# Optimization experiments

Measured on AMD Instinct MI355X. Metric: run time of the kernel, lower is better.

Reference implementation:

```python
import jax, jax.numpy as jnp
import numpy as np

M = 81920          # total triples = 1024 groups * (2*39 + 2)
NB = 39            # num_neighbor
TOTAL_ENT = 14541
TOTAL_REL = 237
D = 100            # embedding_dim == BiLSTM_input_size
H = 100            # lstm hidden (== hidden_size1)
ALPHA = 0.2
MU = 0.001


def _lstm_seq(x, Wih, Whh, b):
    """x: [B,T,D] -> hidden states [B,T,H]. PyTorch gate order i,f,g,o."""
    B = x.shape[0]
    Hh = Whh.shape[1]
    def step(carry, xt):
        h, c = carry
        g = xt @ Wih.T + h @ Whh.T + b
        i, f, gg, o = jnp.split(g, 4, axis=-1)
        c = jax.nn.sigmoid(f) * c + jax.nn.sigmoid(i) * jnp.tanh(gg)
        h = jax.nn.sigmoid(o) * jnp.tanh(c)
        return (h, c), h
    init = (jnp.zeros((B, Hh), x.dtype), jnp.zeros((B, Hh), x.dtype))
    _, hs = jax.lax.scan(step, init, jnp.swapaxes(x, 0, 1))
    return jnp.swapaxes(hs, 0, 1)


def _gat(inp, W, a_vec):
    """inp: [B,N,F] -> [B,F]. GAT-style attention against node 0, thresholded by MU."""
    h = jnp.einsum('bnf,fo->bno', inp, W)
    a0 = jnp.broadcast_to(h[:, :1, :], h.shape)           # node-0 features repeated
    e = jax.nn.leaky_relu(jnp.concatenate([h, a0], axis=-1) @ a_vec, ALPHA)  # [B,N,1]
    att = jax.nn.softmax(e, axis=1)
    att = jnp.maximum(att - MU, 0.0)                      # (x + |x|)/2 == relu(x)
    return jnp.einsum('bnl,bnf->bf', att, h)              # l == 1


def setup_inputs():
    key = jax.random.key(0)
    ks = jax.random.split(key, 20)
    u = 6.0 / np.sqrt(D)        # embedding uniform range as in the module
    sl = 1.0 / np.sqrt(H)       # pytorch LSTM init scale
    F6 = 6 * H
    def uni(k, shape, s):
        return jax.random.uniform(k, shape, minval=-s, maxval=s, dtype=jnp.float32)
    xav1 = 1.414 * np.sqrt(2.0 / (F6 + F6))
    xav2 = 1.414 * np.sqrt(2.0 / (H + H))
    return {
        'batch_h': jax.random.randint(ks[0], (M,), 0, TOTAL_ENT),
        'batch_r': jax.random.randint(ks[1], (M,), 0, TOTAL_REL),
        'batch_t': jax.random.randint(ks[2], (M,), 0, TOTAL_ENT),
        'ent_emb': uni(ks[3], (TOTAL_ENT, D), u),
        'rel_emb': uni(ks[4], (TOTAL_REL, D), u),
        'ent_emb1': uni(ks[5], (TOTAL_ENT, D), u),
        'rel_emb1': uni(ks[6], (TOTAL_REL, D), u),
        'Wih_f': uni(ks[7], (4 * H, D), sl),
        'Whh_f': uni(ks[8], (4 * H, H), sl),
        'b_f': uni(ks[9], (4 * H,), sl),
        'Wih_b': uni(ks[10], (4 * H, D), sl),
        'Whh_b': uni(ks[11], (4 * H, H), sl),
        'b_b': uni(ks[12], (4 * H,), sl),
        'Wih_p': uni(ks[13], (4 * H, D), sl),
        'Whh_p': uni(ks[14], (4 * H, H), sl),
        'b_p': uni(ks[15], (4 * H,), sl),
        'W_att1': jax.random.normal(ks[16], (F6, F6), dtype=jnp.float32) * xav1,
        'a_att1': jax.random.normal(ks[17], (2 * F6, 1), dtype=jnp.float32) * 0.05,
        'W_att2': jax.random.normal(ks[18], (H, H), dtype=jnp.float32) * xav2,
        'a_att2': jax.random.normal(ks[19], (2 * H, 1), dtype=jnp.float32) * 0.05,
    }


def reference(batch_h, batch_r, batch_t, ent_emb, rel_emb, ent_emb1, rel_emb1,
              Wih_f, Whh_f, b_f, Wih_b, Whh_b, b_b, Wih_p, Whh_p, b_p,
              W_att1, a_att1, W_att2, a_att2):
    # triple -> [M,3,D] sequence (head, relation, tail)
    x = jnp.stack([ent_emb[batch_h], rel_emb[batch_r], ent_emb[batch_t]], axis=1)
    # bidirectional LSTM (num_layers=1), zero init states
    of = _lstm_seq(x, Wih_f, Whh_f, b_f)
    ob = _lstm_seq(x[:, ::-1], Wih_b, Whh_b, b_b)[:, ::-1]
    out = jnp.concatenate([of, ob], axis=-1).reshape(x.shape[0], -1)   # [M, 6H]
    out_att = _gat(out.reshape(-1, NB + 1, 6 * H), W_att1, a_att1)     # [M/40, 6H]
    out2 = out.reshape(-1, 2 * NB + 2, 6 * H)                          # [M/80, 80, 6H]
    # second branch: unidirectional ProcessLSTM, last timestep (fc is unused in torch code)
    x1 = jnp.stack([ent_emb1[batch_h], rel_emb1[batch_r], ent_emb1[batch_t]], axis=1)
    op = _lstm_seq(x1, Wih_p, Whh_p, b_p)[:, -1, :]                    # [M, H]
    output_att = _gat(op.reshape(-1, NB + 1, H), W_att2, a_att2)       # [M/40, H]
    op2 = op.reshape(-1, 2 * NB + 2, H)
    return out2[:, 0, :], out_att, op2[:, 0, :], output_att
```

## Files before the change

### kernel.cpp

```cpp
#include <hip/hip_runtime.h>
#include <hip/hip_bf16.h>
#include <cstdint>
#include <cstddef>
#include <cmath>

#define TID ((int)threadIdx.x)

typedef __attribute__((ext_vector_type(8))) short bf16x8;
typedef __attribute__((ext_vector_type(4))) float f32x4;
typedef __attribute__((ext_vector_type(4))) unsigned short us4;
typedef unsigned short ushort_t;

__device__ __forceinline__ float bfu2f(unsigned short u){
    unsigned int x = ((unsigned int)u) << 16; float f; __builtin_memcpy(&f, &x, 4); return f;
}
__device__ __forceinline__ unsigned short f2bu(float f){
    __hip_bfloat16 b = __float2bfloat16(f); unsigned short u; __builtin_memcpy(&u, &b, 2); return u;
}
__device__ __forceinline__ float sigm(float x){
    return __builtin_amdgcn_rcpf(1.0f + __expf(-x));
}
__device__ __forceinline__ float tanhx(float x){
    return 1.0f - 2.0f*__builtin_amdgcn_rcpf(1.0f + __expf(2.0f*x));
}

__global__ __launch_bounds__(256) void k_prep(
    const float* __restrict__ Wih_f, const float* __restrict__ Wih_b, const float* __restrict__ Wih_p,
    const float* __restrict__ Whh_f, const float* __restrict__ Whh_b, const float* __restrict__ Whh_p,
    const float* __restrict__ b_f, const float* __restrict__ b_b, const float* __restrict__ b_p,
    const float* __restrict__ W1, const float* __restrict__ a1,
    const float* __restrict__ W2, const float* __restrict__ a2,
    const float* __restrict__ ent, const float* __restrict__ rel,
    const float* __restrict__ ent1, const float* __restrict__ rel1,
    unsigned short* __restrict__ Asw3, unsigned short* __restrict__ Wsw3,
    float* __restrict__ w1a, float* __restrict__ w1b,
    float* __restrict__ w2a, float* __restrict__ w2b,
    unsigned short* __restrict__ entB, unsigned short* __restrict__ relB,
    unsigned short* __restrict__ ent1B, unsigned short* __restrict__ rel1B)
{
    int bx = blockIdx.x;
    if (bx < 1200){
        int isW = (bx >= 600) ? 1 : 0;
        int e = (bx - isW*600)*256 + TID;
        int l = e/51200, r = e - l*51200;
        int frag = r >> 9, q = r & 511;
        int lanep = q >> 3, j = q & 7;
        int mt = frag >> 2, kt = frag & 3;
        int m = mt*16 + (lanep & 15);
        int f = m >> 2, gg = m & 3;
        int k = kt*32 + (lanep >> 4)*8 + j;
        float v = 0.f;
        if (isW){
            const float* Ws = (l==0)?Wih_f:(l==1)?Wih_b:Wih_p;
            const float* bb = (l==0)?b_f:(l==1)?b_b:b_p;
            if (k < 100)       v = Ws[(gg*100+f)*100 + k];
            else if (k == 100) v = bb[gg*100+f];
        } else {
            const float* Ws = (l==0)?Whh_f:(l==1)?Whh_b:Whh_p;
            if (k < 100)       v = Ws[(gg*100+f)*100 + k];
        }
        (isW ? Wsw3 : Asw3)[e] = f2bu(v);
    } else if (bx < 1375){
        int lane = TID & 63, w = TID >> 6;
        int r = (bx - 1200)*4 + w;
        if (r < 600){
            float x=0.f, y=0.f;
            for (int k=lane;k<600;k+=64){ float wv=W1[r*600+k]; x+=wv*a1[k]; y+=wv*a1[600+k]; }
#pragma unroll
            for (int off=32;off>0;off>>=1){ x+=__shfl_down(x,off,64); y+=__shfl_down(y,off,64); }
            if (lane==0){ w1a[r]=x; w1b[r]=y; }
        } else if (r < 700){
            int f = r-600;
            float x=0.f, y=0.f;
            for (int k=lane;k<100;k+=64){ float wv=W2[f*100+k]; x+=wv*a2[k]; y+=wv*a2[100+k]; }
#pragma unroll
            for (int off=32;off>0;off>>=1){ x+=__shfl_down(x,off,64); y+=__shfl_down(y,off,64); }
            if (lane==0){ w2a[f]=x; w2b[f]=y; }
        }
    } else {
        int e = (bx-1375)*256 + TID;
        if (e < 1454100)            entB[e] = f2bu(ent[e]);
        else if (e < 1477800)       relB[e-1454100] = f2bu(rel[e-1454100]);
        else if (e < 2931900)       ent1B[e-1477800] = f2bu(ent1[e-1477800]);
        else if (e < 2955600)       rel1B[e-2931900] = f2bu(rel1[e-2931900]);
    }
}

__global__ __launch_bounds__(256, 3) void k_lstm(
    const int* __restrict__ bh, const int* __restrict__ br, const int* __restrict__ bt,
    const unsigned short* __restrict__ entB, const unsigned short* __restrict__ relB,
    const unsigned short* __restrict__ ent1B, const unsigned short* __restrict__ rel1B,
    const unsigned short* __restrict__ Asw3, const unsigned short* __restrict__ Wsw3,
    const float* __restrict__ w2a, const float* __restrict__ w2b,
    unsigned short* __restrict__ out6, float* __restrict__ z2,
    float* __restrict__ out0, float* __restrict__ op0)
{
    __shared__ __align__(16) ushort_t XA[48][136];
    __shared__ __align__(16) ushort_t HA2[2][48][136];
    __shared__ float S0o[600];
    __shared__ float S0p[100];
    __shared__ float sc2[40], tc2[40], att2[40];
    __shared__ int sidx[3][40];

    int g = blockIdx.x, m0 = g*40;
    if (TID < 40){
        sidx[0][TID] = bh[m0+TID];
        sidx[1][TID] = br[m0+TID];
        sidx[2][TID] = bt[m0+TID];
    }
    {
        us4 zz; zz[0]=0; zz[1]=0; zz[2]=0; zz[3]=0;
        for (int i=TID; i<1632; i+=256) ((us4*)XA)[i] = zz;
        for (int i=TID; i<3264; i+=256) ((us4*)HA2)[i] = zz;
    }
    __syncthreads();
    if (TID < 48) XA[TID][100] = 0x3F80;
    __syncthreads();

    int lane = TID & 63;
    int wid  = TID >> 6;
    int l15  = lane & 15;
    int quad = lane >> 4;
    int nmt  = (wid==0) ? 7 : 6;
    bool doS0 = ((g & 1) == 0);
    int rrow = g >> 1;

    float c[21];
    us4 xreg[4];

#pragma unroll
    for (int j=0;j<4;j++){
        int idx = TID + j*256;
        if (idx < 1000){
            int s = idx/25, ch = idx - s*25;
            xreg[j] = *(const us4*)(entB + (size_t)sidx[0][s]*100 + ch*4);
        }
    }

    int prevc = -1;
    for (int k=0; k<9; k++){
        int l = k/3, t = k - l*3;
        const ushort_t* Aswl = Asw3 + l*51200;
        const ushort_t* Wswl = Wsw3 + l*51200;
        ushort_t (*hr)[136] = HA2[k & 1];
        ushort_t (*hw)[136] = HA2[(k+1) & 1];

#pragma unroll
        for (int j=0;j<4;j++){
            int idx = TID + j*256;
            if (idx < 1000){
                int s = idx/25, ch = idx - s*25;
                *(us4*)&XA[s][ch*4] = xreg[j];
            }
        }
        if (prevc >= 0){
            unsigned short* base = out6 + (size_t)prevc*8192000 + (size_t)m0*100;
#pragma unroll
            for (int j=0;j<4;j++){
                int idx = TID + j*256;
                if (idx < 1000){
                    int s = idx/25, ch = idx - s*25;
                    *(us4*)(base + s*100 + ch*4) = *(const us4*)&hr[s][ch*4];
                }
            }
        }
        if (k < 8){
            int ln = (k+1)/3, tn = (k+1) - ln*3;
            int pn = (ln==1) ? (2-tn) : tn;
            const ushort_t* tb = (ln==2) ? ((pn==1)? rel1B : ent1B)
                                         : ((pn==1)? relB  : entB);
#pragma unroll
            for (int j=0;j<4;j++){
                int idx = TID + j*256;
                if (idx < 1000){
                    int s = idx/25, ch = idx - s*25;
                    xreg[j] = *(const us4*)(tb + (size_t)sidx[pn][s]*100 + ch*4);
                }
            }
        }
        __syncthreads();

        int wbase = (l==0) ? t*200 : (l==1) ? (2-t)*200 + 100 : 0;
#pragma unroll
        for (int i=0;i<7;i++){
            if (i < nmt){
                int mt = wid + 4*i;
                bf16x8 ax[4], ah[4];
#pragma unroll
                for (int kt=0;kt<4;kt++)
                    ax[kt] = *(const bf16x8*)(Wswl + ((mt*4+kt)*64 + lane)*8);
                if (t > 0){
#pragma unroll
                    for (int kt=0;kt<4;kt++)
                        ah[kt] = *(const bf16x8*)(Aswl + ((mt*4+kt)*64 + lane)*8);
                }
                int f = mt*4 + quad;
#pragma unroll
                for (int nt=0;nt<3;nt++){
                    f32x4 acc = (f32x4){0.f,0.f,0.f,0.f};
#pragma unroll
                    for (int kt=0;kt<4;kt++){
                        bf16x8 xf = *(const bf16x8*)&XA[nt*16 + l15][kt*32 + quad*8];
                        acc = __builtin_amdgcn_mfma_f32_16x16x32_bf16(ax[kt], xf, acc, 0, 0, 0);
                    }
                    if (t > 0){
#pragma unroll
                        for (int kt=0;kt<4;kt++){
                            bf16x8 hf = *(const bf16x8*)&hr[nt*16 + l15][kt*32 + quad*8];
                            acc = __builtin_amdgcn_mfma_f32_16x16x32_bf16(ah[kt], hf, acc, 0, 0, 0);
                        }
                    }
                    int s = nt*16 + l15;
                    bool valid = (nt < 2) || (l15 < 8);
                    float cp = (t==0) ? 0.f : c[i*3+nt];
                    float cn = sigm(acc[1])*cp + sigm(acc[0])*tanhx(acc[2]);
                    float h  = sigm(acc[3])*tanhx(cn);
                    c[i*3+nt] = cn;
                    if (valid){
                        hw[s][f] = f2bu(h);
                        if (doS0 && s==0){
                            if (l < 2)        S0o[wbase + f] = h;
                            else if (t == 2)  S0p[f] = h;
                        }
                    }
                }
            }
        }
        prevc = (l < 2) ? (l*3 + t) : -1;
        __syncthreads();
    }
    ushort_t (*hf)[136] = HA2[1];

    for (int n = wid; n < 40; n += 4){
        float a2=0.f, b2=0.f;
        for (int k=lane;k<100;k+=64){ float v=bfu2f(hf[n][k]); a2 += v*w2a[k]; b2 += v*w2b[k]; }
#pragma unroll
        for (int off=32; off>0; off>>=1){ a2 += __shfl_down(a2,off,64); b2 += __shfl_down(b2,off,64); }
        if (lane==0){ sc2[n]=a2; tc2[n]=b2; }
    }
    __syncthreads();
    if (wid == 0){
        float e = -1e30f;
        if (lane < 40){
            float x = sc2[lane] + tc2[0];
            e = (x > 0.f) ? x : 0.2f*x;
        }
        float mx = e;
#pragma unroll
        for (int off=32;off>0;off>>=1) mx = fmaxf(mx, __shfl_down(mx,off,64));
        mx = __shfl(mx, 0, 64);
        float pexp = (lane<40) ? __expf(e-mx) : 0.f;
        float sm = pexp;
#pragma unroll
        for (int off=32;off>0;off>>=1) sm += __shfl_down(sm,off,64);
        sm = __shfl(sm, 0, 64);
        if (lane < 40){
            float a = pexp/sm - 0.001f;
            att2[lane] = (a > 0.f) ? a : 0.f;
        }
    }
    __syncthreads();
    for (int j=TID; j<100; j+=256){
        float acc = 0.f;
#pragma unroll
        for (int n=0;n<40;n++) acc += att2[n]*bfu2f(hf[n][j]);
        z2[(size_t)g*100 + j] = acc;
    }
    if (doS0){
        for (int j=TID; j<600; j+=256) out0[(size_t)rrow*600 + j] = S0o[j];
        for (int j=TID; j<100; j+=256) op0[(size_t)rrow*100 + j] = S0p[j];
    }
}

__global__ __launch_bounds__(256, 3) void k_att(const unsigned short* __restrict__ out6,
    const float* __restrict__ w1a, const float* __restrict__ w1b, float* __restrict__ z)
{
    __shared__ __align__(16) ushort_t RL[40][600];
    __shared__ float sc1[40], tc1[40], att1[40];
    int g = blockIdx.x, m0 = g*40;
#pragma unroll
    for (int cc=0; cc<6; cc++){
        int l = cc/3, t = cc - l*3;
        int sb = (l==0) ? t*200 : (2-t)*200 + 100;
        const unsigned short* base = out6 + (size_t)cc*8192000 + (size_t)m0*100;
        for (int idx=TID; idx<1000; idx+=256){
            int s = idx/25, ch = idx - s*25;
            *(us4*)&RL[s][sb + ch*4] = *(const us4*)(base + s*100 + ch*4);
        }
    }
    __syncthreads();
    int lane = TID & 63, wid = TID >> 6;
    for (int n = wid; n < 40; n += 4){
        float a=0.f, b=0.f;
        for (int k=lane;k<600;k+=64){ float v=bfu2f(RL[n][k]); a += v*w1a[k]; b += v*w1b[k]; }
#pragma unroll
        for (int off=32; off>0; off>>=1){ a += __shfl_down(a,off,64); b += __shfl_down(b,off,64); }
        if (lane==0){ sc1[n]=a; tc1[n]=b; }
    }
    __syncthreads();
    if (wid == 0){
        float e = -1e30f;
        if (lane < 40){
            float x = sc1[lane] + tc1[0];
            e = (x > 0.f) ? x : 0.2f*x;
        }
        float mx = e;
#pragma unroll
        for (int off=32;off>0;off>>=1) mx = fmaxf(mx, __shfl_down(mx,off,64));
        mx = __shfl(mx, 0, 64);
        float pexp = (lane<40) ? __expf(e-mx) : 0.f;
        float sm = pexp;
#pragma unroll
        for (int off=32;off>0;off>>=1) sm += __shfl_down(sm,off,64);
        sm = __shfl(sm, 0, 64);
        if (lane < 40){
            float a = pexp/sm - 0.001f;
            att1[lane] = (a > 0.f) ? a : 0.f;
        }
    }
    __syncthreads();
    for (int j=TID; j<600; j+=256){
        float acc = 0.f;
#pragma unroll
        for (int n=0;n<40;n++) acc += att1[n]*bfu2f(RL[n][j]);
        z[(size_t)g*600 + j] = acc;
    }
}

__global__ __launch_bounds__(256) void k_post(const float* __restrict__ z, const float* __restrict__ z2,
    const float* __restrict__ W1, const float* __restrict__ W2,
    float* __restrict__ oatt, float* __restrict__ oatt2)
{
    extern __shared__ float zl[];
    int y = blockIdx.y;
    const float* zz = (y==3)? z2 : z;
    const float* W  = (y==3)? W2 : W1;
    float* o        = (y==3)? oatt2 : oatt;
    int dim         = (y==3)? 100 : 600;
    int rb = blockIdx.x*16;
    for (int r=0;r<16;r++){
        for (int j=TID;j<dim;j+=256) zl[r*dim+j] = zz[(size_t)(rb+r)*dim + j];
    }
    __syncthreads();
    int cc = (y==3)? TID : y*256 + TID;
    if (cc < dim){
        float acc[16];
#pragma unroll
        for (int r=0;r<16;r++) acc[r]=0.f;
        for (int k=0;k<dim;k++){
            float w = W[(size_t)k*dim + cc];
#pragma unroll
            for (int r=0;r<16;r++) acc[r] += zl[r*dim+k]*w;
        }
        for (int r=0;r<16;r++) o[(size_t)(rb+r)*dim + cc] = acc[r];
    }
}

__global__ void k_sentinel(float* o, float v){ o[0] = v; }

extern "C" void kernel_launch(void* const* d_in, const int* in_sizes, int n_in,
                              void* d_out, int out_size, void* d_ws, size_t ws_size,
                              hipStream_t stream)
{
    const int*   bh   = (const int*)d_in[0];
    const int*   br   = (const int*)d_in[1];
    const int*   bt   = (const int*)d_in[2];
    const float* ent  = (const float*)d_in[3];
    const float* rel  = (const float*)d_in[4];
    const float* ent1 = (const float*)d_in[5];
    const float* rel1 = (const float*)d_in[6];
    const float* Wih_f = (const float*)d_in[7];
    const float* Whh_f = (const float*)d_in[8];
    const float* b_f   = (const float*)d_in[9];
    const float* Wih_b = (const float*)d_in[10];
    const float* Whh_b = (const float*)d_in[11];
    const float* b_b   = (const float*)d_in[12];
    const float* Wih_p = (const float*)d_in[13];
    const float* Whh_p = (const float*)d_in[14];
    const float* b_p   = (const float*)d_in[15];
    const float* W1 = (const float*)d_in[16];
    const float* a1 = (const float*)d_in[17];
    const float* W2 = (const float*)d_in[18];
    const float* a2 = (const float*)d_in[19];

    char* wsb = (char*)d_ws;
    size_t off = 0;
    auto alloc = [&](size_t bytes) -> char* {
        char* p = wsb + off;
        off += (bytes + 255) & ~(size_t)255;
        return p;
    };
    unsigned short* entB  = (unsigned short*)alloc((size_t)1454100*2);
    unsigned short* relB  = (unsigned short*)alloc((size_t)23700*2);
    unsigned short* ent1B = (unsigned short*)alloc((size_t)1454100*2);
    unsigned short* rel1B = (unsigned short*)alloc((size_t)23700*2);
    unsigned short* Asw3  = (unsigned short*)alloc((size_t)153600*2);
    unsigned short* Wsw3  = (unsigned short*)alloc((size_t)153600*2);
    float* w1a = (float*)alloc(600*4);
    float* w1b = (float*)alloc(600*4);
    float* w2a = (float*)alloc(100*4);
    float* w2b = (float*)alloc(100*4);
    float* z   = (float*)alloc((size_t)2048*600*4);
    float* z2  = (float*)alloc((size_t)2048*100*4);
    unsigned short* out6 = (unsigned short*)alloc((size_t)49152000*2);

    float* dout  = (float*)d_out;
    float* out0  = dout;
    float* oatt  = dout + 614400;
    float* op0   = dout + 1843200;
    float* oatt2 = dout + 1945600;

    if (ws_size < off){
        k_sentinel<<<1,1,0,stream>>>(dout, (float)ws_size);
        return;
    }

    k_prep<<<12923, 256, 0, stream>>>(Wih_f, Wih_b, Wih_p, Whh_f, Whh_b, Whh_p,
                                      b_f, b_b, b_p, W1, a1, W2, a2,
                                      ent, rel, ent1, rel1,
                                      Asw3, Wsw3, w1a, w1b, w2a, w2b,
                                      entB, relB, ent1B, rel1B);

    k_lstm<<<2048, 256, 0, stream>>>(bh, br, bt, entB, relB, ent1B, rel1B,
                                     Asw3, Wsw3, w2a, w2b, out6, z2, out0, op0);

    k_att<<<2048, 256, 0, stream>>>(out6, w1a, w1b, z);

    k_post<<<dim3(128,4), 256, 16*600*4, stream>>>(z, z2, W1, W2, oatt, oatt2);
}
```

Measured before the change: 513.1 us.

## Widen LSTM blocks to 512 threads and reorder MFMA loop for operand reuse

The LSTM kernel now runs 8 waves per block instead of 4, so each wave handles 3-4 gate tiles rather than 6-7. The MFMA loop is restructured to put the k-tile outermost, so each X/H fragment loaded from LDS is reused across all of a wave's M-tiles, with accumulators held in registers. LDS buffers shrink from 48 to 40 rows and out-of-range rows are clamped. Launch bounds rise to (512,4), which tightens the register budget for the larger accumulator array and risks spills.

```diff
diff --git a/kernel.cpp b/kernel.cpp
--- a/kernel.cpp
+++ b/kernel.cpp
@@ -86,7 +86,7 @@
     }
 }
 
-__global__ __launch_bounds__(256, 3) void k_lstm(
+__global__ __launch_bounds__(512, 4) void k_lstm(
     const int* __restrict__ bh, const int* __restrict__ br, const int* __restrict__ bt,
     const unsigned short* __restrict__ entB, const unsigned short* __restrict__ relB,
     const unsigned short* __restrict__ ent1B, const unsigned short* __restrict__ rel1B,
@@ -95,8 +95,8 @@
     unsigned short* __restrict__ out6, float* __restrict__ z2,
     float* __restrict__ out0, float* __restrict__ op0)
 {
-    __shared__ __align__(16) ushort_t XA[48][136];
-    __shared__ __align__(16) ushort_t HA2[2][48][136];
+    __shared__ __align__(16) ushort_t XA[40][136];
+    __shared__ __align__(16) ushort_t HA2[2][40][136];
     __shared__ float S0o[600];
     __shared__ float S0p[100];
     __shared__ float sc2[40], tc2[40], att2[40];
@@ -110,27 +110,30 @@
     }
     {
         us4 zz; zz[0]=0; zz[1]=0; zz[2]=0; zz[3]=0;
-        for (int i=TID; i<1632; i+=256) ((us4*)XA)[i] = zz;
-        for (int i=TID; i<3264; i+=256) ((us4*)HA2)[i] = zz;
-    }
-    __syncthreads();
-    if (TID < 48) XA[TID][100] = 0x3F80;
+        for (int i=TID; i<1360; i+=512) ((us4*)XA)[i] = zz;
+        for (int i=TID; i<2720; i+=512) ((us4*)HA2)[i] = zz;
+    }
+    __syncthreads();
+    if (TID < 40) XA[TID][100] = 0x3F80;
     __syncthreads();
 
     int lane = TID & 63;
-    int wid  = TID >> 6;
+    int w    = TID >> 6;
     int l15  = lane & 15;
     int quad = lane >> 4;
-    int nmt  = (wid==0) ? 7 : 6;
+    int nmt  = (w==0) ? 4 : 3;
     bool doS0 = ((g & 1) == 0);
     int rrow = g >> 1;
-
-    float c[21];
-    us4 xreg[4];
-
-#pragma unroll
-    for (int j=0;j<4;j++){
-        int idx = TID + j*256;
+    int rwB[3];
+#pragma unroll
+    for (int nt=0;nt<3;nt++){ int r = nt*16 + l15; rwB[nt] = (r > 39) ? 39 : r; }
+
+    float c[12];
+    us4 xreg[2];
+
+#pragma unroll
+    for (int j=0;j<2;j++){
+        int idx = TID + j*512;
         if (idx < 1000){
             int s = idx/25, ch = idx - s*25;
             xreg[j] = *(const us4*)(entB + (size_t)sidx[0][s]*100 + ch*4);
@@ -146,8 +149,8 @@
         ushort_t (*hw)[136] = HA2[(k+1) & 1];
 
 #pragma unroll
-        for (int j=0;j<4;j++){
-            int idx = TID + j*256;
+        for (int j=0;j<2;j++){
+            int idx = TID + j*512;
             if (idx < 1000){
                 int s = idx/25, ch = idx - s*25;
                 *(us4*)&XA[s][ch*4] = xreg[j];
@@ -156,8 +159,8 @@
         if (prevc >= 0){
             unsigned short* base = out6 + (size_t)prevc*8192000 + (size_t)m0*100;
 #pragma unroll
-            for (int j=0;j<4;j++){
-                int idx = TID + j*256;
+            for (int j=0;j<2;j++){
+                int idx = TID + j*512;
                 if (idx < 1000){
                     int s = idx/25, ch = idx - s*25;
                     *(us4*)(base + s*100 + ch*4) = *(const us4*)&hr[s][ch*4];
@@ -170,8 +173,8 @@
             const ushort_t* tb = (ln==2) ? ((pn==1)? rel1B : ent1B)
                                          : ((pn==1)? relB  : entB);
 #pragma unroll
-            for (int j=0;j<4;j++){
-                int idx = TID + j*256;
+            for (int j=0;j<2;j++){
+                int idx = TID + j*512;
                 if (idx < 1000){
                     int s = idx/25, ch = idx - s*25;
                     xreg[j] = *(const us4*)(tb + (size_t)sidx[pn][s]*100 + ch*4);
@@ -180,41 +183,51 @@
         }
         __syncthreads();
 
+        f32x4 acc[4][3];
+#pragma unroll
+        for (int i=0;i<4;i++)
+#pragma unroll
+            for (int nt=0;nt<3;nt++) acc[i][nt] = (f32x4){0.f,0.f,0.f,0.f};
+
+#pragma unroll
+        for (int kt=0; kt<4; kt++){
+            bf16x8 bx[3], bhh[3];
+#pragma unroll
+            for (int nt=0;nt<3;nt++){
+                bx[nt] = *(const bf16x8*)&XA[rwB[nt]][kt*32 + quad*8];
+                if (t > 0) bhh[nt] = *(const bf16x8*)&hr[rwB[nt]][kt*32 + quad*8];
+            }
+#pragma unroll
+            for (int i=0;i<4;i++){
+                if (i < nmt){
+                    int mt = w + 8*i;
+                    bf16x8 ax = *(const bf16x8*)(Wswl + ((mt*4+kt)*64 + lane)*8);
+#pragma unroll
+                    for (int nt=0;nt<3;nt++)
+                        acc[i][nt] = __builtin_amdgcn_mfma_f32_16x16x32_bf16(ax, bx[nt], acc[i][nt], 0, 0, 0);
+                    if (t > 0){
+                        bf16x8 ah = *(const bf16x8*)(Aswl + ((mt*4+kt)*64 + lane)*8);
+#pragma unroll
+                        for (int nt=0;nt<3;nt++)
+                            acc[i][nt] = __builtin_amdgcn_mfma_f32_16x16x32_bf16(ah, bhh[nt], acc[i][nt], 0, 0, 0);
+                    }
+                }
+            }
+        }
+
         int wbase = (l==0) ? t*200 : (l==1) ? (2-t)*200 + 100 : 0;
 #pragma unroll
-        for (int i=0;i<7;i++){
+        for (int i=0;i<4;i++){
             if (i < nmt){
-                int mt = wid + 4*i;
-                bf16x8 ax[4], ah[4];
-#pragma unroll
-                for (int kt=0;kt<4;kt++)
-                    ax[kt] = *(const bf16x8*)(Wswl + ((mt*4+kt)*64 + lane)*8);
-                if (t > 0){
-#pragma unroll
-                    for (int kt=0;kt<4;kt++)
-                        ah[kt] = *(const bf16x8*)(Aswl + ((mt*4+kt)*64 + lane)*8);
-                }
-                int f = mt*4 + quad;
+                int f = (w + 8*i)*4 + quad;
 #pragma unroll
                 for (int nt=0;nt<3;nt++){
-                    f32x4 acc = (f32x4){0.f,0.f,0.f,0.f};
-#pragma unroll
-                    for (int kt=0;kt<4;kt++){
-                        bf16x8 xf = *(const bf16x8*)&XA[nt*16 + l15][kt*32 + quad*8];
-                        acc = __builtin_amdgcn_mfma_f32_16x16x32_bf16(ax[kt], xf, acc, 0, 0, 0);
-                    }
-                    if (t > 0){
-#pragma unroll
-                        for (int kt=0;kt<4;kt++){
-                            bf16x8 hf = *(const bf16x8*)&hr[nt*16 + l15][kt*32 + quad*8];
-                            acc = __builtin_amdgcn_mfma_f32_16x16x32_bf16(ah[kt], hf, acc, 0, 0, 0);
-                        }
-                    }
                     int s = nt*16 + l15;
                     bool valid = (nt < 2) || (l15 < 8);
+                    f32x4 a4 = acc[i][nt];
                     float cp = (t==0) ? 0.f : c[i*3+nt];
-                    float cn = sigm(acc[1])*cp + sigm(acc[0])*tanhx(acc[2]);
-                    float h  = sigm(acc[3])*tanhx(cn);
+                    float cn = sigm(a4[1])*cp + sigm(a4[0])*tanhx(a4[2]);
+                    float h  = sigm(a4[3])*tanhx(cn);
                     c[i*3+nt] = cn;
                     if (valid){
                         hw[s][f] = f2bu(h);
@@ -231,7 +244,7 @@
     }
     ushort_t (*hf)[136] = HA2[1];
 
-    for (int n = wid; n < 40; n += 4){
+    for (int n = w; n < 40; n += 8){
         float a2=0.f, b2=0.f;
         for (int k=lane;k<100;k+=64){ float v=bfu2f(hf[n][k]); a2 += v*w2a[k]; b2 += v*w2b[k]; }
 #pragma unroll
@@ -239,7 +252,7 @@
         if (lane==0){ sc2[n]=a2; tc2[n]=b2; }
     }
     __syncthreads();
-    if (wid == 0){
+    if (w == 0){
         float e = -1e30f;
         if (lane < 40){
             float x = sc2[lane] + tc2[0];
@@ -260,15 +273,15 @@
         }
     }
     __syncthreads();
-    for (int j=TID; j<100; j+=256){
+    if (TID < 100){
         float acc = 0.f;
 #pragma unroll
-        for (int n=0;n<40;n++) acc += att2[n]*bfu2f(hf[n][j]);
-        z2[(size_t)g*100 + j] = acc;
+        for (int n=0;n<40;n++) acc += att2[n]*bfu2f(hf[n][TID]);
+        z2[(size_t)g*100 + TID] = acc;
     }
     if (doS0){
-        for (int j=TID; j<600; j+=256) out0[(size_t)rrow*600 + j] = S0o[j];
-        for (int j=TID; j<100; j+=256) op0[(size_t)rrow*100 + j] = S0p[j];
+        for (int j=TID; j<600; j+=512) out0[(size_t)rrow*600 + j] = S0o[j];
+        if (TID < 100) op0[(size_t)rrow*100 + TID] = S0p[TID];
     }
 }
 
@@ -421,7 +434,7 @@
                                       Asw3, Wsw3, w1a, w1b, w2a, w2b,
                                       entB, relB, ent1B, rel1B);
 
-    k_lstm<<<2048, 256, 0, stream>>>(bh, br, bt, entB, relB, ent1B, rel1B,
+    k_lstm<<<2048, 512, 0, stream>>>(bh, br, bt, entB, relB, ent1B, rel1B,
                                      Asw3, Wsw3, w2a, w2b, out6, z2, out0, op0);
 
     k_att<<<2048, 256, 0, stream>>>(out6, w1a, w1b, z);
```

New measurement: 610.7 us. +19.0%, slower.
